# Kernel tuning notes

Hardware: AMD Instinct MI355X
Metric: run time of the kernel (lower is better)

## Reference

```python
import jax, jax.numpy as jnp
import numpy as np

MAX_DISPLACEMENT = 4  # matches init_kwargs
EPS = 1e-12  # torch F.normalize clamp


def _l2_normalize(x):
    # L2 normalize over channel dim (axis=1), matching torch.nn.functional.normalize
    n = jnp.sqrt(jnp.sum(x * x, axis=1, keepdims=True))
    return x / jnp.maximum(n, EPS)


def setup_inputs() -> dict:
    key = jax.random.key(0)
    k1, k2 = jax.random.split(key)
    B, C, H, W = 16, 256, 64, 64
    fA = jax.random.normal(k1, (B, C, H, W), dtype=jnp.float32)
    fB = jax.random.normal(k2, (B, C, H, W), dtype=jnp.float32)
    return {"fA": fA, "fB": fB}


def reference(fA, fB):
    d = MAX_DISPLACEMENT
    B, C, H, W = fA.shape
    fAn = _l2_normalize(fA)
    fBn = _l2_normalize(fB)
    # zero-pad fB by d (matches F.unfold padding=d), then take shifted windows.
    fBp = jnp.pad(fBn, ((0, 0), (0, 0), (d, d), (d, d)))
    outs = []
    # Fixed structural loop over (2d+1)^2 = 81 displacements (row-major ky, kx,
    # matching F.unfold's kernel-position ordering). No huge patch tensor is
    # materialized; each term is a channel dot-product of fA with shifted fB.
    for dy in range(2 * d + 1):
        for dx in range(2 * d + 1):
            shifted = jax.lax.dynamic_slice(
                fBp, (0, 0, dy, dx), (B, C, H, W))
            outs.append(jnp.sum(fAn * shifted, axis=1))  # (B, H, W)
    return jnp.stack(outs, axis=1)  # (B, (2d+1)^2, H, W)
```

## Files before the change

kernel.cpp:

```cpp
#include <hip/hip_runtime.h>
#include <hip/hip_bf16.h>
#include <math.h>

typedef short short8 __attribute__((ext_vector_type(8)));
typedef float f32x16 __attribute__((ext_vector_type(16)));

#define BB 16
#define CC 256
#define HH 64
#define WW 64
#define HWX 4096
#define DD 4
#define KD 9
#define KK 81
#define NSLOT 10

__device__ __forceinline__ short bf16c(float x) {
    __hip_bfloat16 h = __float2bfloat16(x);
    return *reinterpret_cast<short*>(&h);
}

__device__ __forceinline__ void b_issue32(const float* __restrict__ row,
                                          int c0, int l, float* v) {
    #pragma unroll
    for (int j = 0; j < 32; ++j)
        v[j] = row[(size_t)(c0 + j) * HWX + l];
}

__device__ __forceinline__ void b_commit32(const float* v, unsigned short* bufp,
                                           float* partp, int c0, int wvslot, int l) {
    float ss = 0.f;
    #pragma unroll
    for (int j = 0; j < 32; ++j) ss += v[j] * v[j];
    #pragma unroll
    for (int ch = 0; ch < 4; ++ch) {
        short8 st;
        #pragma unroll
        for (int j = 0; j < 8; ++j) st[j] = bf16c(v[ch * 8 + j]);
        const int c = c0 + ch * 8;
        const int byte = (l * 512 + c * 2) ^ ((l & 31) << 4);
        *(short8*)((char*)bufp + byte) = st;
    }
    partp[wvslot * 64 + l] = ss;
}

__global__ __launch_bounds__(512) void corr_mfma(
    const float* __restrict__ fA, const float* __restrict__ fB,
    float* __restrict__ out)
{
    __shared__ __attribute__((aligned(16))) unsigned short buf[2][WW * CC];
    __shared__ float red[2][2][KD][WW + 1];
    __shared__ float part[2][8 * WW];
    __shared__ float invA_ls[2][WW];

    const int bid = blockIdx.x;
    const int swzb = (bid & 7) * 64 + (bid >> 3);
    const int b = swzb >> 5, jr = swzb & 31;
    const int h0 = 2 * jr;

    const int tid = threadIdx.x;
    const int l = tid & 63;
    const int wvu = __builtin_amdgcn_readfirstlane(tid >> 6);
    const int g = wvu >> 2;
    const int q = wvu & 3;
    const int hg = h0 + g;
    const int ti = q >> 1, tj = q & 1;
    const int ml = l & 31, kg = l >> 5;
    const int m = ti * 32 + ml;
    const int n = tj * 32 + ml;

    const float* Abase = fA + (size_t)b * CC * HWX + hg * WW;
    {
        float ss = 0.f;
        #pragma unroll
        for (int r = 0; r < 8; ++r) {
            const int c = q * 64 + r * 8;
            float v[8]; short8 st;
            #pragma unroll
            for (int j = 0; j < 8; ++j) v[j] = Abase[(size_t)(c + j) * HWX + l];
            #pragma unroll
            for (int j = 0; j < 8; ++j) ss += v[j] * v[j];
            #pragma unroll
            for (int j = 0; j < 8; ++j) st[j] = bf16c(v[j]);
            const int byte = (l * 512 + c * 2) ^ ((l & 31) << 4);
            *(short8*)((char*)buf[g] + byte) = st;
        }
        part[1][wvu * 64 + l] = ss;
    }
    for (int i = tid; i < 2 * 2 * KD * (WW + 1); i += 512) ((float*)red)[i] = 0.f;
    __syncthreads();
    if (tid < 2 * WW) {
        const int gg = tid >> 6, ll = tid & 63;
        float s = part[1][(gg * 4 + 0) * 64 + ll] + part[1][(gg * 4 + 1) * 64 + ll]
                + part[1][(gg * 4 + 2) * 64 + ll] + part[1][(gg * 4 + 3) * 64 + ll];
        invA_ls[gg][ll] = 1.f / fmaxf(sqrtf(s), 1e-12f);
    }
    short8 afr[16];
    #pragma unroll
    for (int s = 0; s < 16; ++s) {
        const int byte = (m * 512 + s * 32 + kg * 16) ^ ((m & 31) << 4);
        afr[s] = *(const short8*)((const char*)buf[g] + byte);
    }
    __syncthreads();

    const float* fBb = fB + (size_t)b * CC * HWX;
    {
        const int hb0 = h0 - DD;
        if ((unsigned)hb0 < HH) {
            float v[32];
            b_issue32(fBb + (size_t)hb0 * WW, wvu * 32, l, v);
            b_commit32(v, buf[0], part[0], wvu * 32, wvu, l);
        }
    }
    __syncthreads();

    for (int r = 0; r < NSLOT; ++r) {
        const int cur = r & 1;
        const int hb = h0 - DD + r;
        const bool vcur = (unsigned)hb < HH;
        const bool vnext = (r + 1 < NSLOT) && ((unsigned)(hb + 1) < HH);
        const int dy = r - g;
        const bool dyv = (dy >= 0 && dy < KD);
        const bool comp = dyv && vcur;

        float v[32];
        if (vnext) b_issue32(fBb + (size_t)(hb + 1) * WW, wvu * 32, l, v);

        if (r >= 1) {
            const int dyp = (r - 1) - g;
            if (dyp >= 0 && dyp < KD) {
                float* ob = out + (((size_t)b * KK + dyp * KD) * HH + hg) * WW;
                ob[(size_t)q * HWX + l] = red[g][cur ^ 1][q][l];
                ob[(size_t)(q + 4) * HWX + l] = red[g][cur ^ 1][q + 4][l];
                if (q == 0) ob[(size_t)8 * HWX + l] = red[g][cur ^ 1][8][l];
            }
        }

        if (comp) {
            f32x16 acc;
            #pragma unroll
            for (int i = 0; i < 16; ++i) acc[i] = 0.f;
            __builtin_amdgcn_s_setprio(1);
            #pragma unroll
            for (int s = 0; s < 16; ++s) {
                const int byte = (n * 512 + s * 32 + kg * 16) ^ ((n & 31) << 4);
                short8 bfr = *(const short8*)((const char*)buf[cur] + byte);
                acc = __builtin_amdgcn_mfma_f32_32x32x16_bf16(afr[s], bfr, acc, 0, 0, 0);
            }
            __builtin_amdgcn_s_setprio(0);
            float sB = 0.f;
            #pragma unroll
            for (int qq = 0; qq < 8; ++qq) sB += part[cur][qq * 64 + n];
            const float ibn = 1.f / fmaxf(sqrtf(sB), 1e-12f);
            #pragma unroll
            for (int rr = 0; rr < 16; ++rr) {
                const int w = ti * 32 + (rr & 3) + 8 * (rr >> 2) + 4 * kg;
                const int dx = n - w + 4;
                if (dx >= 0 && dx < KD)
                    red[g][cur][dx][w] = acc[rr] * ibn * invA_ls[g][w];
            }
        } else if (dyv) {
            #pragma unroll
            for (int rr = 0; rr < 16; ++rr) {
                const int w = ti * 32 + (rr & 3) + 8 * (rr >> 2) + 4 * kg;
                const int dx = n - w + 4;
                if (dx >= 0 && dx < KD) red[g][cur][dx][w] = 0.f;
            }
        }

        if (vnext)
            b_commit32(v, buf[cur ^ 1], part[cur ^ 1], wvu * 32, wvu, l);
        __syncthreads();
    }

    {
        const int dyp = (NSLOT - 1) - g;
        if (dyp >= 0 && dyp < KD) {
            const int par = (NSLOT - 1) & 1;
            float* ob = out + (((size_t)b * KK + dyp * KD) * HH + hg) * WW;
            ob[(size_t)q * HWX + l] = red[g][par][q][l];
            ob[(size_t)(q + 4) * HWX + l] = red[g][par][q + 4][l];
            if (q == 0) ob[(size_t)8 * HWX + l] = red[g][par][8][l];
        }
    }
}

extern "C" void kernel_launch(void* const* d_in, const int* in_sizes, int n_in,
                              void* d_out, int out_size, void* d_ws, size_t ws_size,
                              hipStream_t stream) {
    const float* fA = (const float*)d_in[0];
    const float* fB = (const float*)d_in[1];
    float* outp = (float*)d_out;
    corr_mfma<<<dim3(BB * HH / 2), 512, 0, stream>>>(fA, fB, outp);
}
```

Measured before the change: 66.40 us.

## Vectorize fB row loads to float4 and switch LDS to channel-group-major layout

The fB row loader now issues 16-byte float4 global loads (8 channels x 4 pixels per lane) instead of 32 scalar 4-byte loads. To fit this, the LDS tile layout becomes channel-group-major (1 KB per group of 8 channels) with a new XOR swizzle. The per-pixel squared-norm partials are reduced across lanes with shuffles before being written. The aim is fewer global memory instructions and wider transactions, at the cost of extra shuffles and possibly different LDS bank-conflict behaviour on the MFMA operand reads.

Result: no change. 66.43 us (+0.0%).

```diff
diff --git a/kernel.cpp b/kernel.cpp
--- a/kernel.cpp
+++ b/kernel.cpp
@@ -4,6 +4,7 @@
 
 typedef short short8 __attribute__((ext_vector_type(8)));
 typedef float f32x16 __attribute__((ext_vector_type(16)));
+typedef float f32x4  __attribute__((ext_vector_type(4)));
 
 #define BB 16
 #define CC 256
@@ -20,28 +21,47 @@
     return *reinterpret_cast<short*>(&h);
 }
 
-__device__ __forceinline__ void b_issue32(const float* __restrict__ row,
-                                          int c0, int l, float* v) {
-    #pragma unroll
-    for (int j = 0; j < 32; ++j)
-        v[j] = row[(size_t)(c0 + j) * HWX + l];
-}
-
-__device__ __forceinline__ void b_commit32(const float* v, unsigned short* bufp,
-                                           float* partp, int c0, int wvslot, int l) {
-    float ss = 0.f;
-    #pragma unroll
-    for (int j = 0; j < 32; ++j) ss += v[j] * v[j];
-    #pragma unroll
-    for (int ch = 0; ch < 4; ++ch) {
+__device__ __forceinline__ int bl_byte(int c8, int w) {
+    int byte = c8 * 1024 + w * 16;
+    return byte ^ (((byte >> 10) & 3) << 4);
+}
+
+__device__ __forceinline__ void b_issue(const float* __restrict__ row,
+                                        int wvu, int l, f32x4* v4) {
+    const float* p = row + (size_t)(wvu * 32 + (l >> 4) * 8) * HWX + 4 * (l & 15);
+    #pragma unroll
+    for (int ch = 0; ch < 8; ++ch)
+        v4[ch] = *(const f32x4*)(p + (size_t)ch * HWX);
+}
+
+__device__ __forceinline__ void b_commit(const f32x4* v4, unsigned short* bufp,
+                                         float* partp, int wvu, int l) {
+    const int c8 = wvu * 4 + (l >> 4);
+    float sswi[4];
+    #pragma unroll
+    for (int wi = 0; wi < 4; ++wi) {
         short8 st;
+        float ss = 0.f;
         #pragma unroll
-        for (int j = 0; j < 8; ++j) st[j] = bf16c(v[ch * 8 + j]);
-        const int c = c0 + ch * 8;
-        const int byte = (l * 512 + c * 2) ^ ((l & 31) << 4);
-        *(short8*)((char*)bufp + byte) = st;
-    }
-    partp[wvslot * 64 + l] = ss;
+        for (int ch = 0; ch < 8; ++ch) {
+            float x = v4[ch][wi];
+            ss += x * x;
+            st[ch] = bf16c(x);
+        }
+        *(short8*)((char*)bufp + bl_byte(c8, 4 * (l & 15) + wi)) = st;
+        sswi[wi] = ss;
+    }
+    #pragma unroll
+    for (int wi = 0; wi < 4; ++wi) {
+        float s = sswi[wi];
+        s += __shfl_xor(s, 16, 64);
+        s += __shfl_xor(s, 32, 64);
+        sswi[wi] = s;
+    }
+    if ((l >> 4) == 0) {
+        f32x4 p4; p4[0] = sswi[0]; p4[1] = sswi[1]; p4[2] = sswi[2]; p4[3] = sswi[3];
+        *(f32x4*)&partp[wvu * 64 + 4 * l] = p4;
+    }
 }
 
 __global__ __launch_bounds__(512) void corr_mfma(
@@ -82,8 +102,7 @@
             for (int j = 0; j < 8; ++j) ss += v[j] * v[j];
             #pragma unroll
             for (int j = 0; j < 8; ++j) st[j] = bf16c(v[j]);
-            const int byte = (l * 512 + c * 2) ^ ((l & 31) << 4);
-            *(short8*)((char*)buf[g] + byte) = st;
+            *(short8*)((char*)buf[g] + bl_byte(q * 8 + r, l)) = st;
         }
         part[1][wvu * 64 + l] = ss;
     }
@@ -97,19 +116,17 @@
     }
     short8 afr[16];
     #pragma unroll
-    for (int s = 0; s < 16; ++s) {
-        const int byte = (m * 512 + s * 32 + kg * 16) ^ ((m & 31) << 4);
-        afr[s] = *(const short8*)((const char*)buf[g] + byte);
-    }
+    for (int s = 0; s < 16; ++s)
+        afr[s] = *(const short8*)((const char*)buf[g] + bl_byte(s * 2 + kg, m));
     __syncthreads();
 
     const float* fBb = fB + (size_t)b * CC * HWX;
     {
         const int hb0 = h0 - DD;
         if ((unsigned)hb0 < HH) {
-            float v[32];
-            b_issue32(fBb + (size_t)hb0 * WW, wvu * 32, l, v);
-            b_commit32(v, buf[0], part[0], wvu * 32, wvu, l);
+            f32x4 v4[8];
+            b_issue(fBb + (size_t)hb0 * WW, wvu, l, v4);
+            b_commit(v4, buf[0], part[0], wvu, l);
         }
     }
     __syncthreads();
@@ -123,8 +140,8 @@
         const bool dyv = (dy >= 0 && dy < KD);
         const bool comp = dyv && vcur;
 
-        float v[32];
-        if (vnext) b_issue32(fBb + (size_t)(hb + 1) * WW, wvu * 32, l, v);
+        f32x4 v4[8];
+        if (vnext) b_issue(fBb + (size_t)(hb + 1) * WW, wvu, l, v4);
 
         if (r >= 1) {
             const int dyp = (r - 1) - g;
@@ -143,8 +160,7 @@
             __builtin_amdgcn_s_setprio(1);
             #pragma unroll
             for (int s = 0; s < 16; ++s) {
-                const int byte = (n * 512 + s * 32 + kg * 16) ^ ((n & 31) << 4);
-                short8 bfr = *(const short8*)((const char*)buf[cur] + byte);
+                short8 bfr = *(const short8*)((const char*)buf[cur] + bl_byte(s * 2 + kg, n));
                 acc = __builtin_amdgcn_mfma_f32_32x32x16_bf16(afr[s], bfr, acc, 0, 0, 0);
             }
             __builtin_amdgcn_s_setprio(0);
@@ -169,7 +185,7 @@
         }
 
         if (vnext)
-            b_commit32(v, buf[cur ^ 1], part[cur ^ 1], wvu * 32, wvu, l);
+            b_commit(v4, buf[cur ^ 1], part[cur ^ 1], wvu, l);
         __syncthreads();
     }
 
```

## Split B-row prefetch into halves interleaved with MFMA and write outputs directly

Applied to the files above, without the earlier changes.

Removes the LDS staging buffer for results and writes correlation values straight from MFMA accumulators to global memory, zero-filling the out-of-range border entries explicitly. The fA inverse norm is folded into the A fragments once, which drops a per-output multiply. The next fB row is now loaded and committed in two 16-channel halves interleaved between the two halves of the MFMA loop, which lowers register pressure and overlaps global loads with compute. The per-iteration __syncthreads is replaced by a raw LDS-waitcnt plus barrier. In exchange, the global stores are scattered and less coalesced, and the A fragments take an extra bf16 rounding step.

New measurement: 60.06 us, median of 3. 1.11x faster.

```diff
diff --git a/kernel.cpp b/kernel.cpp
--- a/kernel.cpp
+++ b/kernel.cpp
@@ -15,33 +15,40 @@
 #define KK 81
 #define NSLOT 10
 
+#define RAW_BAR() do { \
+    asm volatile("s_waitcnt lgkmcnt(0)" ::: "memory"); \
+    __builtin_amdgcn_s_barrier(); \
+} while (0)
+
 __device__ __forceinline__ short bf16c(float x) {
     __hip_bfloat16 h = __float2bfloat16(x);
     return *reinterpret_cast<short*>(&h);
 }
 
-__device__ __forceinline__ void b_issue32(const float* __restrict__ row,
+__device__ __forceinline__ int lds_byte(int w, int c) {
+    return (w * 512 + c * 2) ^ ((w & 31) << 4);
+}
+
+__device__ __forceinline__ void b_issue16(const float* __restrict__ row,
                                           int c0, int l, float* v) {
     #pragma unroll
-    for (int j = 0; j < 32; ++j)
+    for (int j = 0; j < 16; ++j)
         v[j] = row[(size_t)(c0 + j) * HWX + l];
 }
 
-__device__ __forceinline__ void b_commit32(const float* v, unsigned short* bufp,
-                                           float* partp, int c0, int wvslot, int l) {
+__device__ __forceinline__ float b_commit16(const float* v, unsigned short* bufp,
+                                            int c0, int l) {
     float ss = 0.f;
     #pragma unroll
-    for (int j = 0; j < 32; ++j) ss += v[j] * v[j];
-    #pragma unroll
-    for (int ch = 0; ch < 4; ++ch) {
+    for (int j = 0; j < 16; ++j) ss += v[j] * v[j];
+    #pragma unroll
+    for (int h = 0; h < 2; ++h) {
         short8 st;
         #pragma unroll
-        for (int j = 0; j < 8; ++j) st[j] = bf16c(v[ch * 8 + j]);
-        const int c = c0 + ch * 8;
-        const int byte = (l * 512 + c * 2) ^ ((l & 31) << 4);
-        *(short8*)((char*)bufp + byte) = st;
-    }
-    partp[wvslot * 64 + l] = ss;
+        for (int j = 0; j < 8; ++j) st[j] = bf16c(v[h * 8 + j]);
+        *(short8*)((char*)bufp + lds_byte(l, c0 + h * 8)) = st;
+    }
+    return ss;
 }
 
 __global__ __launch_bounds__(512) void corr_mfma(
@@ -49,7 +56,6 @@
     float* __restrict__ out)
 {
     __shared__ __attribute__((aligned(16))) unsigned short buf[2][WW * CC];
-    __shared__ float red[2][2][KD][WW + 1];
     __shared__ float part[2][8 * WW];
     __shared__ float invA_ls[2][WW];
 
@@ -82,12 +88,10 @@
             for (int j = 0; j < 8; ++j) ss += v[j] * v[j];
             #pragma unroll
             for (int j = 0; j < 8; ++j) st[j] = bf16c(v[j]);
-            const int byte = (l * 512 + c * 2) ^ ((l & 31) << 4);
-            *(short8*)((char*)buf[g] + byte) = st;
+            *(short8*)((char*)buf[g] + lds_byte(l, c)) = st;
         }
         part[1][wvu * 64 + l] = ss;
     }
-    for (int i = tid; i < 2 * 2 * KD * (WW + 1); i += 512) ((float*)red)[i] = 0.f;
     __syncthreads();
     if (tid < 2 * WW) {
         const int gg = tid >> 6, ll = tid & 63;
@@ -97,19 +101,34 @@
     }
     short8 afr[16];
     #pragma unroll
-    for (int s = 0; s < 16; ++s) {
-        const int byte = (m * 512 + s * 32 + kg * 16) ^ ((m & 31) << 4);
-        afr[s] = *(const short8*)((const char*)buf[g] + byte);
-    }
+    for (int s = 0; s < 16; ++s)
+        afr[s] = *(const short8*)((const char*)buf[g] + lds_byte(m, s * 16 + kg * 8));
     __syncthreads();
-
+    {
+        const float iam = invA_ls[g][m];
+        #pragma unroll
+        for (int s = 0; s < 16; ++s) {
+            short8 t = afr[s];
+            #pragma unroll
+            for (int j = 0; j < 8; ++j) {
+                union { unsigned u; float f; } uu;
+                uu.u = ((unsigned)(unsigned short)t[j]) << 16;
+                t[j] = bf16c(uu.f * iam);
+            }
+            afr[s] = t;
+        }
+    }
     const float* fBb = fB + (size_t)b * CC * HWX;
     {
         const int hb0 = h0 - DD;
         if ((unsigned)hb0 < HH) {
-            float v[32];
-            b_issue32(fBb + (size_t)hb0 * WW, wvu * 32, l, v);
-            b_commit32(v, buf[0], part[0], wvu * 32, wvu, l);
+            const float* row = fBb + (size_t)hb0 * WW;
+            float v[16];
+            b_issue16(row, wvu * 32, l, v);
+            float ss = b_commit16(v, buf[0], wvu * 32, l);
+            b_issue16(row, wvu * 32 + 16, l, v);
+            ss += b_commit16(v, buf[0], wvu * 32 + 16, l);
+            part[0][wvu * 64 + l] = ss;
         }
     }
     __syncthreads();
@@ -122,29 +141,36 @@
         const int dy = r - g;
         const bool dyv = (dy >= 0 && dy < KD);
         const bool comp = dyv && vcur;
-
-        float v[32];
-        if (vnext) b_issue32(fBb + (size_t)(hb + 1) * WW, wvu * 32, l, v);
-
-        if (r >= 1) {
-            const int dyp = (r - 1) - g;
-            if (dyp >= 0 && dyp < KD) {
-                float* ob = out + (((size_t)b * KK + dyp * KD) * HH + hg) * WW;
-                ob[(size_t)q * HWX + l] = red[g][cur ^ 1][q][l];
-                ob[(size_t)(q + 4) * HWX + l] = red[g][cur ^ 1][q + 4][l];
-                if (q == 0) ob[(size_t)8 * HWX + l] = red[g][cur ^ 1][8][l];
-            }
-        }
-
+        const float* nrow = fBb + (size_t)(hb + 1) * WW;
+        float* ob = out + (((size_t)b * KK + dy * KD) * HH + hg) * WW;
+
+        float v[16];
+        if (vnext) b_issue16(nrow, wvu * 32, l, v);
+
+        f32x16 acc;
         if (comp) {
-            f32x16 acc;
             #pragma unroll
             for (int i = 0; i < 16; ++i) acc[i] = 0.f;
             __builtin_amdgcn_s_setprio(1);
             #pragma unroll
-            for (int s = 0; s < 16; ++s) {
-                const int byte = (n * 512 + s * 32 + kg * 16) ^ ((n & 31) << 4);
-                short8 bfr = *(const short8*)((const char*)buf[cur] + byte);
+            for (int s = 0; s < 8; ++s) {
+                short8 bfr = *(const short8*)((const char*)buf[cur] + lds_byte(n, s * 16 + kg * 8));
+                acc = __builtin_amdgcn_mfma_f32_32x32x16_bf16(afr[s], bfr, acc, 0, 0, 0);
+            }
+            __builtin_amdgcn_s_setprio(0);
+        }
+
+        float ssn = 0.f;
+        if (vnext) {
+            ssn = b_commit16(v, buf[cur ^ 1], wvu * 32, l);
+            b_issue16(nrow, wvu * 32 + 16, l, v);
+        }
+
+        if (comp) {
+            __builtin_amdgcn_s_setprio(1);
+            #pragma unroll
+            for (int s = 8; s < 16; ++s) {
+                short8 bfr = *(const short8*)((const char*)buf[cur] + lds_byte(n, s * 16 + kg * 8));
                 acc = __builtin_amdgcn_mfma_f32_32x32x16_bf16(afr[s], bfr, acc, 0, 0, 0);
             }
             __builtin_amdgcn_s_setprio(0);
@@ -157,31 +183,30 @@
                 const int w = ti * 32 + (rr & 3) + 8 * (rr >> 2) + 4 * kg;
                 const int dx = n - w + 4;
                 if (dx >= 0 && dx < KD)
-                    red[g][cur][dx][w] = acc[rr] * ibn * invA_ls[g][w];
+                    ob[(size_t)dx * HWX + w] = acc[rr] * ibn;
+            }
+            if (q == 3) {
+                int i = -1;
+                if (l < 10) i = l;
+                else if (l >= 16 && l < 26) i = l - 16;
+                if (i >= 0) {
+                    const int wz0 = (i < 4) ? 0 : (i < 7) ? 1 : (i < 9) ? 2 : 3;
+                    const int dx0 = i - ((wz0 == 0) ? 0 : (wz0 == 1) ? 4 : (wz0 == 2) ? 7 : 9);
+                    const int wz = (l < 10) ? wz0 : 63 - wz0;
+                    const int dxz = (l < 10) ? dx0 : 8 - dx0;
+                    ob[(size_t)dxz * HWX + wz] = 0.f;
+                }
             }
         } else if (dyv) {
-            #pragma unroll
-            for (int rr = 0; rr < 16; ++rr) {
-                const int w = ti * 32 + (rr & 3) + 8 * (rr >> 2) + 4 * kg;
-                const int dx = n - w + 4;
-                if (dx >= 0 && dx < KD) red[g][cur][dx][w] = 0.f;
-            }
-        }
-
-        if (vnext)
-            b_commit32(v, buf[cur ^ 1], part[cur ^ 1], wvu * 32, wvu, l);
-        __syncthreads();
-    }
-
-    {
-        const int dyp = (NSLOT - 1) - g;
-        if (dyp >= 0 && dyp < KD) {
-            const int par = (NSLOT - 1) & 1;
-            float* ob = out + (((size_t)b * KK + dyp * KD) * HH + hg) * WW;
-            ob[(size_t)q * HWX + l] = red[g][par][q][l];
-            ob[(size_t)(q + 4) * HWX + l] = red[g][par][q + 4][l];
-            if (q == 0) ob[(size_t)8 * HWX + l] = red[g][par][8][l];
-        }
+            for (int i = q * 64 + l; i < KD * WW; i += 256)
+                ob[(size_t)(i >> 6) * HWX + (i & 63)] = 0.f;
+        }
+
+        if (vnext) {
+            ssn += b_commit16(v, buf[cur ^ 1], wvu * 32 + 16, l);
+            part[cur ^ 1][wvu * 64 + l] = ssn;
+        }
+        RAW_BAR();
     }
 }
 
```
